# Optimization experiments

Measured on AMD Instinct MI355X. Metric: run time of the kernel, lower is better.

The kernel has to match this reference:

```python
import jax, jax.numpy as jnp
import numpy as np

N_NODES = 50000
N_EDGES = 800000
IN_F = 128
OUT_F = 128
EDGE_F = 6


def setup_inputs() -> dict:
    key = jax.random.key(0)
    k1, k2, k3, k4, k5, k6, k7 = jax.random.split(key, 7)
    nodeFeatures = jax.random.normal(k1, (N_NODES, IN_F), dtype=jnp.float32)
    edgeIndex = jax.random.randint(k2, (N_EDGES, 2), 0, N_NODES, dtype=jnp.int64)
    edgeFeatures = jax.random.normal(k3, (N_EDGES, EDGE_F), dtype=jnp.float32)
    # nn.Linear params (kaiming-uniform-ish init scale)
    lim_n = 1.0 / np.sqrt(IN_F)
    lim_e = 1.0 / np.sqrt(EDGE_F)
    W = jax.random.uniform(k4, (IN_F, OUT_F), minval=-lim_n, maxval=lim_n, dtype=jnp.float32)
    b = jax.random.uniform(k5, (OUT_F,), minval=-lim_n, maxval=lim_n, dtype=jnp.float32)
    We = jax.random.uniform(k6, (EDGE_F, OUT_F), minval=-lim_e, maxval=lim_e, dtype=jnp.float32)
    be = jax.random.uniform(k7, (OUT_F,), minval=-lim_e, maxval=lim_e, dtype=jnp.float32)
    return {"nodeFeatures": nodeFeatures, "edgeIndex": edgeIndex,
            "edgeFeatures": edgeFeatures, "W": W, "b": b, "We": We, "be": be}


def reference(nodeFeatures, edgeIndex, edgeFeatures, W, b, We, be):
    # node linear: [N, out]
    transformed = nodeFeatures @ W + b
    # edge linear: [E, out]
    edgeMsg = edgeFeatures @ We + be
    src = edgeIndex[:, 0]
    dst = edgeIndex[:, 1]
    # per-edge message = transformed[src] + edgeMsg, scatter-add into dst
    messages = transformed[src] + edgeMsg  # [E, out]
    aggregated = jax.ops.segment_sum(messages, dst, num_segments=nodeFeatures.shape[0])
    return jax.nn.relu(aggregated)
```

## Files before the change

kernel.cpp:

```cpp
#include <hip/hip_runtime.h>
#include <hip/hip_bf16.h>
#include <stdint.h>

#define IN_F 128
#define EDGE_F 6
#define TILE_E 4096
#define NBIN_PAD 256

using bf16x8 = __attribute__((ext_vector_type(8))) short;
using f32x4  = __attribute__((ext_vector_type(4))) float;

__device__ __forceinline__ float bf2f(unsigned short u) {
    return __uint_as_float(((unsigned int)u) << 16);
}
__device__ __forceinline__ unsigned short f2bfbits(float f) {
    __hip_bfloat16 h = __float2bfloat16(f);
    return *reinterpret_cast<unsigned short*>(&h);
}
__device__ __forceinline__ unsigned int packbf(float a, float b) {
    return ((unsigned int)f2bfbits(b) << 16) | (unsigned int)f2bfbits(a);
}

__global__ __launch_bounds__(256) void pack_hist_cast(
        const int* __restrict__ eidx, const float* __restrict__ ef,
        uint4* __restrict__ efp, unsigned short* __restrict__ pmat,
        int n_edges, int nblk_e, int n_cast, int eb,
        const float* __restrict__ nf, unsigned short* __restrict__ nfb,
        const float* __restrict__ W, const float* __restrict__ b,
        const float* __restrict__ We, const float* __restrict__ be,
        unsigned short* __restrict__ Wpack, float* __restrict__ W2pack) {
    const int tid = threadIdx.x;
    const int blk = blockIdx.x;
    __shared__ int hist[NBIN_PAD];

    if (blk == eb) {
        for (int idx = tid; idx < 16384; idx += 256) {
            int j = idx & 7, lane = (idx >> 3) & 63, ft = (idx >> 9) & 7, kb = idx >> 12;
            int k = kb * 32 + (lane >> 4) * 8 + j;
            int f = ft * 16 + (lane & 15);
            Wpack[idx] = f2bfbits(W[k * 128 + f]);
        }
        for (int idx = tid; idx < 1024; idx += 256) {
            int j = idx >> 7, f = idx & 127;
            float w = 0.f;
            if (j < 6)       w = We[j * 128 + f];
            else if (j == 6) w = b[f] + be[f];
            W2pack[idx] = w;
        }
    } else {
        const bool hb = (blk < nblk_e);
        if (hb) {
            hist[tid] = 0;
            __syncthreads();
        }
        const int t = blk * 256 + tid;
        if (t < n_edges) {
            const int2 pr = reinterpret_cast<const int2*>(eidx)[t];
            const float2* efs = reinterpret_cast<const float2*>(ef + (size_t)t * EDGE_F);
            const float2 f0 = efs[0], f1 = efs[1], f2 = efs[2];
            uint4 q;
            q.x = (unsigned int)pr.x | ((unsigned int)pr.y << 16);
            q.y = packbf(f0.x, f0.y);
            q.z = packbf(f1.x, f1.y);
            q.w = packbf(f2.x, f2.y);
            efp[t] = q;
        }
        if (hb) {
            const int e0 = blk * TILE_E;
#pragma unroll
            for (int i = 0; i < TILE_E / 256; ++i) {
                const int e = e0 + i * 256 + tid;
                if (e < n_edges) {
                    const int dst = reinterpret_cast<const int2*>(eidx)[e].y;
                    atomicAdd(&hist[dst >> 8], 1);
                }
            }
            __syncthreads();
            pmat[(size_t)blk * NBIN_PAD + tid] = (unsigned short)hist[tid];
        }
    }
    const int t = blk * 256 + tid;
    const int stride = gridDim.x * 256;
    for (int i = t; i < n_cast; i += stride) {
        const float4 lo = reinterpret_cast<const float4*>(nf)[2 * i];
        const float4 hi = reinterpret_cast<const float4*>(nf)[2 * i + 1];
        uint4 o;
        o.x = packbf(lo.x, lo.y); o.y = packbf(lo.z, lo.w);
        o.z = packbf(hi.x, hi.y); o.w = packbf(hi.z, hi.w);
        reinterpret_cast<uint4*>(nfb)[i] = o;
    }
}

__global__ __launch_bounds__(256) void coarse_scatter(
        const uint4* __restrict__ efp, const unsigned short* __restrict__ pmat,
        uint4* __restrict__ rec_c, int* __restrict__ gbase,
        int n_edges, int nblk_e, int nbin) {
    const int tid = threadIdx.x;
    const int blk = blockIdx.x;
    __shared__ int cur[NBIN_PAD];
    __shared__ int sc[NBIN_PAD];
    int tot = 0, pre = 0;
#pragma unroll 4
    for (int bb = 0; bb < nblk_e; ++bb) {
        const int v = pmat[(size_t)bb * NBIN_PAD + tid];
        tot += v;
        pre += (bb < blk) ? v : 0;
    }
    sc[tid] = tot;
    __syncthreads();
    for (int off = 1; off < 256; off <<= 1) {
        int t2 = (tid >= off) ? sc[tid - off] : 0;
        __syncthreads();
        sc[tid] += t2;
        __syncthreads();
    }
    const int excl = sc[tid] - tot;
    cur[tid] = excl + pre;
    if (blk == 0 && tid <= nbin) gbase[tid] = excl;
    __syncthreads();
    const int e0 = blk * TILE_E;
#pragma unroll
    for (int i = 0; i < TILE_E / 256; ++i) {
        const int e = e0 + i * 256 + tid;
        if (e < n_edges) {
            const uint4 q = efp[e];
            const int cb = q.x >> 24;
            const int pos = atomicAdd(&cur[cb], 1);
            rec_c[pos] = q;
        }
    }
}

__global__ __launch_bounds__(256) void fine_rank(
        const uint4* __restrict__ rec_c, const int* __restrict__ gbase,
        uint4* __restrict__ rec, int* __restrict__ rowptr, int n_nodes) {
    const int tid = threadIdx.x;
    const int c = blockIdx.x;
    const int rbase = gbase[c], rend = gbase[c + 1];
    __shared__ int fcnt[256];
    __shared__ int fpos[256];
    fcnt[tid] = 0;
    __syncthreads();
    for (int i = rbase + tid; i < rend; i += 256) {
        const unsigned int qx = reinterpret_cast<const unsigned int*>(rec_c)[(size_t)i * 4];
        atomicAdd(&fcnt[(qx >> 16) & 255], 1);
    }
    __syncthreads();
    const int own = fcnt[tid];
    for (int off = 1; off < 256; off <<= 1) {
        int t2 = (tid >= off) ? fcnt[tid - off] : 0;
        __syncthreads();
        fcnt[tid] += t2;
        __syncthreads();
    }
    const int excl = fcnt[tid] - own;
    fpos[tid] = excl;
    const int n = c * 256 + tid;
    if (n <= n_nodes) rowptr[n] = rbase + excl;
    if (c == 0 && tid == 0) rowptr[n_nodes] = gbase[gridDim.x];
    __syncthreads();
    for (int i = rbase + tid; i < rend; i += 256) {
        const uint4 q = rec_c[i];
        const int r = atomicAdd(&fpos[(q.x >> 16) & 255], 1);
        rec[rbase + r] = q;
    }
}

__global__ __launch_bounds__(256) void aggregate_bf16(
        const unsigned short* __restrict__ nfb, const uint4* __restrict__ rec,
        const int* __restrict__ rowptr, unsigned short* __restrict__ S,
        unsigned short* __restrict__ E8, int n_nodes) {
    const int lane = threadIdx.x & 63;
    const int wv = __builtin_amdgcn_readfirstlane(threadIdx.x >> 6);
    const int n = blockIdx.x * 4 + wv;
    if (n >= n_nodes) return;
    const int r0 = rowptr[n], r1 = rowptr[n + 1];
    const int deg = r1 - r0;
    float ax = 0.f, ay = 0.f;
    float e0 = 0.f, e1 = 0.f, e2 = 0.f, e3 = 0.f, e4 = 0.f, e5 = 0.f;
    int i = r0;
    for (; i + 7 < r1; i += 8) {
        uint4 q[8];
        unsigned int u[8];
#pragma unroll
        for (int j = 0; j < 8; ++j) q[j] = rec[i + j];
#pragma unroll
        for (int j = 0; j < 8; ++j)
            u[j] = reinterpret_cast<const unsigned int*>(nfb + (size_t)(q[j].x & 0xFFFFu) * IN_F)[lane];
#pragma unroll
        for (int j = 0; j < 8; ++j) {
            ax += bf2f((unsigned short)u[j]);
            ay += bf2f((unsigned short)(u[j] >> 16));
            e0 += bf2f((unsigned short)q[j].y);
            e1 += bf2f((unsigned short)(q[j].y >> 16));
            e2 += bf2f((unsigned short)q[j].z);
            e3 += bf2f((unsigned short)(q[j].z >> 16));
            e4 += bf2f((unsigned short)q[j].w);
            e5 += bf2f((unsigned short)(q[j].w >> 16));
        }
    }
    for (; i + 3 < r1; i += 4) {
        uint4 q[4];
        unsigned int u[4];
#pragma unroll
        for (int j = 0; j < 4; ++j) q[j] = rec[i + j];
#pragma unroll
        for (int j = 0; j < 4; ++j)
            u[j] = reinterpret_cast<const unsigned int*>(nfb + (size_t)(q[j].x & 0xFFFFu) * IN_F)[lane];
#pragma unroll
        for (int j = 0; j < 4; ++j) {
            ax += bf2f((unsigned short)u[j]);
            ay += bf2f((unsigned short)(u[j] >> 16));
            e0 += bf2f((unsigned short)q[j].y);
            e1 += bf2f((unsigned short)(q[j].y >> 16));
            e2 += bf2f((unsigned short)q[j].z);
            e3 += bf2f((unsigned short)(q[j].z >> 16));
            e4 += bf2f((unsigned short)q[j].w);
            e5 += bf2f((unsigned short)(q[j].w >> 16));
        }
    }
    for (; i < r1; ++i) {
        const uint4 q0 = rec[i];
        const unsigned int u0 = reinterpret_cast<const unsigned int*>(nfb + (size_t)(q0.x & 0xFFFFu) * IN_F)[lane];
        ax += bf2f((unsigned short)u0); ay += bf2f((unsigned short)(u0 >> 16));
        e0 += bf2f((unsigned short)q0.y); e1 += bf2f((unsigned short)(q0.y >> 16));
        e2 += bf2f((unsigned short)q0.z); e3 += bf2f((unsigned short)(q0.z >> 16));
        e4 += bf2f((unsigned short)q0.w); e5 += bf2f((unsigned short)(q0.w >> 16));
    }
    unsigned short* row = S + (size_t)n * IN_F;
    reinterpret_cast<unsigned int*>(row)[lane] = packbf(ax, ay);
    if (lane == 0) {
        uint4 q;
        q.x = packbf(e0, e1);
        q.y = packbf(e2, e3);
        q.z = packbf(e4, e5);
        q.w = packbf((float)deg, 0.f);
        *reinterpret_cast<uint4*>(E8 + (size_t)n * 8) = q;
    }
}

__global__ __launch_bounds__(256) void gemm_mfma(
        const unsigned short* __restrict__ S, const unsigned short* __restrict__ E8,
        const unsigned short* __restrict__ Wpack, const float* __restrict__ W2pack,
        float* __restrict__ out, int n_nodes) {
    __shared__ __align__(16) short Wl[16384];
    __shared__ float W2l[1024];
    const int tid = threadIdx.x;
    for (int i = tid; i < 2048; i += 256)
        reinterpret_cast<uint4*>(Wl)[i] = reinterpret_cast<const uint4*>(Wpack)[i];
    for (int i = tid; i < 1024; i += 256) W2l[i] = W2pack[i];

    const int wv = tid >> 6, lane = tid & 63;
    const int m = lane & 15, quad = lane >> 4;
    const int n0 = blockIdx.x * 64 + wv * 16;

    const int arow = min(n0 + m, n_nodes - 1);
    const unsigned short* ap = S + (size_t)arow * IN_F + quad * 8;
    bf16x8 a[4];
#pragma unroll
    for (int kb = 0; kb < 4; ++kb)
        a[kb] = *reinterpret_cast<const bf16x8*>(ap + kb * 32);

    __syncthreads();

    f32x4 acc[8];
#pragma unroll
    for (int ft = 0; ft < 8; ++ft) acc[ft] = (f32x4){0.f, 0.f, 0.f, 0.f};

#pragma unroll
    for (int kb = 0; kb < 4; ++kb) {
#pragma unroll
        for (int ft = 0; ft < 8; ++ft) {
            const bf16x8 bfrag =
                reinterpret_cast<const bf16x8*>(Wl)[(kb * 8 + ft) * 64 + lane];
            acc[ft] = __builtin_amdgcn_mfma_f32_16x16x32_bf16(a[kb], bfrag, acc[ft], 0, 0, 0);
        }
    }

    float e[4][7];
#pragma unroll
    for (int r = 0; r < 4; ++r) {
        const int n = min(n0 + quad * 4 + r, n_nodes - 1);
        const uint4 q = *reinterpret_cast<const uint4*>(E8 + (size_t)n * 8);
        e[r][0] = bf2f((unsigned short)q.x); e[r][1] = bf2f((unsigned short)(q.x >> 16));
        e[r][2] = bf2f((unsigned short)q.y); e[r][3] = bf2f((unsigned short)(q.y >> 16));
        e[r][4] = bf2f((unsigned short)q.z); e[r][5] = bf2f((unsigned short)(q.z >> 16));
        e[r][6] = bf2f((unsigned short)q.w);
    }
#pragma unroll
    for (int ft = 0; ft < 8; ++ft) {
        const int f = ft * 16 + m;
        float w2[7];
#pragma unroll
        for (int j = 0; j < 7; ++j) w2[j] = W2l[j * 128 + f];
#pragma unroll
        for (int r = 0; r < 4; ++r) {
            const int n = n0 + quad * 4 + r;
            if (n < n_nodes) {
                float v = acc[ft][r];
#pragma unroll
                for (int j = 0; j < 7; ++j) v += e[r][j] * w2[j];
                out[(size_t)n * 128 + f] = fmaxf(v, 0.f);
            }
        }
    }
}

extern "C" void kernel_launch(void* const* d_in, const int* in_sizes, int n_in,
                              void* d_out, int out_size, void* d_ws, size_t ws_size,
                              hipStream_t stream) {
    const float* nf = (const float*)d_in[0];
    const int* eidx = (const int*)d_in[1];
    const float* ef = (const float*)d_in[2];
    const float* W  = (const float*)d_in[3];
    const float* b  = (const float*)d_in[4];
    const float* We = (const float*)d_in[5];
    const float* be = (const float*)d_in[6];
    float* out = (float*)d_out;

    const int n_nodes = in_sizes[0] / IN_F;
    const int n_edges = in_sizes[1] / 2;

    const int eb = (n_edges + 255) / 256;
    const int nblk_e = (n_edges + TILE_E - 1) / TILE_E;
    const int nbin = (n_nodes + 255) >> 8;
    const int n_cast = n_nodes * (IN_F / 8);

    uint4* rec   = (uint4*)d_ws;
    uint4* efp   = rec + n_edges;
    uint4* rec_c = efp + n_edges;
    unsigned short* S = (unsigned short*)(rec_c + n_edges);
    unsigned short* E8 = S + (size_t)n_nodes * IN_F;
    unsigned short* Wpack = E8 + (size_t)n_nodes * 8;
    float* W2pack = (float*)(Wpack + 16384);
    unsigned short* pmat = (unsigned short*)(W2pack + 1024);
    int* gbase  = (int*)(pmat + (size_t)nblk_e * NBIN_PAD);
    int* rowptr = gbase + 260;
    const int rp_pad = (n_nodes + 1 + 3) & ~3;
    unsigned short* nfb = (unsigned short*)(rowptr + rp_pad);

    pack_hist_cast<<<eb + 1, 256, 0, stream>>>(eidx, ef, efp, pmat,
                                               n_edges, nblk_e, n_cast, eb,
                                               nf, nfb, W, b, We, be, Wpack, W2pack);
    coarse_scatter<<<nblk_e, 256, 0, stream>>>(efp, pmat, rec_c, gbase,
                                               n_edges, nblk_e, nbin);
    fine_rank<<<nbin, 256, 0, stream>>>(rec_c, gbase, rec, rowptr, n_nodes);
    aggregate_bf16<<<(n_nodes + 3) / 4, 256, 0, stream>>>(nfb, rec, rowptr, S, E8, n_nodes);
    gemm_mfma<<<(n_nodes + 63) / 64, 256, 0, stream>>>(S, E8, Wpack, W2pack, out, n_nodes);
}
```

Measured before the change: 194.2 us.

## Fuse fine ranking into aggregation using shared-memory edge index lists

Merges the fine_rank and aggregate kernels into one fine_agg kernel. Each coarse bin of 256 nodes is split across 8 blocks, and each block builds a shared-memory list of 16-bit edge offsets for its 32 nodes. It then gathers rec_c records through those indices instead of writing a fully sorted rec array plus rowptr. This removes one kernel launch and a full global write and read of the 800K sorted records. In exchange, every block rescans the whole bin's record headers twice, and there is a slow fallback path when a block's edge count exceeds the index-buffer capacity.

```diff
diff --git a/kernel.cpp b/kernel.cpp
--- a/kernel.cpp
+++ b/kernel.cpp
@@ -6,6 +6,8 @@
 #define EDGE_F 6
 #define TILE_E 4096
 #define NBIN_PAD 256
+#define SPLIT 8
+#define IDXCAP 1280
 
 using bf16x8 = __attribute__((ext_vector_type(8))) short;
 using f32x4  = __attribute__((ext_vector_type(4))) float;
@@ -131,111 +133,144 @@
     }
 }
 
-__global__ __launch_bounds__(256) void fine_rank(
+__global__ __launch_bounds__(256) void fine_agg(
         const uint4* __restrict__ rec_c, const int* __restrict__ gbase,
-        uint4* __restrict__ rec, int* __restrict__ rowptr, int n_nodes) {
+        const unsigned short* __restrict__ nfb,
+        unsigned short* __restrict__ S, unsigned short* __restrict__ E8,
+        int n_nodes) {
     const int tid = threadIdx.x;
-    const int c = blockIdx.x;
+    const int c = blockIdx.x / SPLIT;
+    const int part = blockIdx.x % SPLIT;
     const int rbase = gbase[c], rend = gbase[c + 1];
-    __shared__ int fcnt[256];
-    __shared__ int fpos[256];
-    fcnt[tid] = 0;
-    __syncthreads();
-    for (int i = rbase + tid; i < rend; i += 256) {
-        const unsigned int qx = reinterpret_cast<const unsigned int*>(rec_c)[(size_t)i * 4];
-        atomicAdd(&fcnt[(qx >> 16) & 255], 1);
-    }
-    __syncthreads();
-    const int own = fcnt[tid];
-    for (int off = 1; off < 256; off <<= 1) {
-        int t2 = (tid >= off) ? fcnt[tid - off] : 0;
+    const int sz = rend - rbase;
+    __shared__ int scnt[32];
+    __shared__ int spos[32];
+    __shared__ int sok;
+    __shared__ unsigned short sidx[IDXCAP];
+    if (tid < 32) scnt[tid] = 0;
+    __syncthreads();
+    for (int i = tid; i < sz; i += 256) {
+        const unsigned int qx =
+            reinterpret_cast<const unsigned int*>(rec_c)[(size_t)(rbase + i) * 4];
+        const int d = (qx >> 16) & 255;
+        if ((d >> 5) == part) atomicAdd(&scnt[d & 31], 1);
+    }
+    __syncthreads();
+    if (tid == 0) {
+        int run = 0;
+        for (int j = 0; j < 32; ++j) { spos[j] = run; run += scnt[j]; }
+        sok = (run <= IDXCAP && sz <= 65535) ? 1 : 0;
+    }
+    __syncthreads();
+    const int ok = sok;
+    if (ok) {
+        for (int i = tid; i < sz; i += 256) {
+            const unsigned int qx =
+                reinterpret_cast<const unsigned int*>(rec_c)[(size_t)(rbase + i) * 4];
+            const int d = (qx >> 16) & 255;
+            if ((d >> 5) == part) {
+                const int r = atomicAdd(&spos[d & 31], 1);
+                sidx[r] = (unsigned short)i;
+            }
+        }
         __syncthreads();
-        fcnt[tid] += t2;
-        __syncthreads();
-    }
-    const int excl = fcnt[tid] - own;
-    fpos[tid] = excl;
-    const int n = c * 256 + tid;
-    if (n <= n_nodes) rowptr[n] = rbase + excl;
-    if (c == 0 && tid == 0) rowptr[n_nodes] = gbase[gridDim.x];
-    __syncthreads();
-    for (int i = rbase + tid; i < rend; i += 256) {
-        const uint4 q = rec_c[i];
-        const int r = atomicAdd(&fpos[(q.x >> 16) & 255], 1);
-        rec[rbase + r] = q;
-    }
-}
-
-__global__ __launch_bounds__(256) void aggregate_bf16(
-        const unsigned short* __restrict__ nfb, const uint4* __restrict__ rec,
-        const int* __restrict__ rowptr, unsigned short* __restrict__ S,
-        unsigned short* __restrict__ E8, int n_nodes) {
-    const int lane = threadIdx.x & 63;
-    const int wv = __builtin_amdgcn_readfirstlane(threadIdx.x >> 6);
-    const int n = blockIdx.x * 4 + wv;
-    if (n >= n_nodes) return;
-    const int r0 = rowptr[n], r1 = rowptr[n + 1];
-    const int deg = r1 - r0;
-    float ax = 0.f, ay = 0.f;
-    float e0 = 0.f, e1 = 0.f, e2 = 0.f, e3 = 0.f, e4 = 0.f, e5 = 0.f;
-    int i = r0;
-    for (; i + 7 < r1; i += 8) {
-        uint4 q[8];
-        unsigned int u[8];
-#pragma unroll
-        for (int j = 0; j < 8; ++j) q[j] = rec[i + j];
-#pragma unroll
-        for (int j = 0; j < 8; ++j)
-            u[j] = reinterpret_cast<const unsigned int*>(nfb + (size_t)(q[j].x & 0xFFFFu) * IN_F)[lane];
-#pragma unroll
-        for (int j = 0; j < 8; ++j) {
-            ax += bf2f((unsigned short)u[j]);
-            ay += bf2f((unsigned short)(u[j] >> 16));
-            e0 += bf2f((unsigned short)q[j].y);
-            e1 += bf2f((unsigned short)(q[j].y >> 16));
-            e2 += bf2f((unsigned short)q[j].z);
-            e3 += bf2f((unsigned short)(q[j].z >> 16));
-            e4 += bf2f((unsigned short)q[j].w);
-            e5 += bf2f((unsigned short)(q[j].w >> 16));
-        }
-    }
-    for (; i + 3 < r1; i += 4) {
-        uint4 q[4];
-        unsigned int u[4];
-#pragma unroll
-        for (int j = 0; j < 4; ++j) q[j] = rec[i + j];
-#pragma unroll
-        for (int j = 0; j < 4; ++j)
-            u[j] = reinterpret_cast<const unsigned int*>(nfb + (size_t)(q[j].x & 0xFFFFu) * IN_F)[lane];
-#pragma unroll
-        for (int j = 0; j < 4; ++j) {
-            ax += bf2f((unsigned short)u[j]);
-            ay += bf2f((unsigned short)(u[j] >> 16));
-            e0 += bf2f((unsigned short)q[j].y);
-            e1 += bf2f((unsigned short)(q[j].y >> 16));
-            e2 += bf2f((unsigned short)q[j].z);
-            e3 += bf2f((unsigned short)(q[j].z >> 16));
-            e4 += bf2f((unsigned short)q[j].w);
-            e5 += bf2f((unsigned short)(q[j].w >> 16));
-        }
-    }
-    for (; i < r1; ++i) {
-        const uint4 q0 = rec[i];
-        const unsigned int u0 = reinterpret_cast<const unsigned int*>(nfb + (size_t)(q0.x & 0xFFFFu) * IN_F)[lane];
-        ax += bf2f((unsigned short)u0); ay += bf2f((unsigned short)(u0 >> 16));
-        e0 += bf2f((unsigned short)q0.y); e1 += bf2f((unsigned short)(q0.y >> 16));
-        e2 += bf2f((unsigned short)q0.z); e3 += bf2f((unsigned short)(q0.z >> 16));
-        e4 += bf2f((unsigned short)q0.w); e5 += bf2f((unsigned short)(q0.w >> 16));
-    }
-    unsigned short* row = S + (size_t)n * IN_F;
-    reinterpret_cast<unsigned int*>(row)[lane] = packbf(ax, ay);
-    if (lane == 0) {
-        uint4 q;
-        q.x = packbf(e0, e1);
-        q.y = packbf(e2, e3);
-        q.z = packbf(e4, e5);
-        q.w = packbf((float)deg, 0.f);
-        *reinterpret_cast<uint4*>(E8 + (size_t)n * 8) = q;
+    }
+    const int lane = tid & 63;
+    const int wv = tid >> 6;
+#pragma unroll 1
+    for (int k = 0; k < 8; ++k) {
+        const int dl = part * 32 + wv * 8 + k;
+        const int n = c * 256 + dl;
+        if (n >= n_nodes) continue;
+        float ax = 0.f, ay = 0.f;
+        float e0 = 0.f, e1 = 0.f, e2 = 0.f, e3 = 0.f, e4 = 0.f, e5 = 0.f;
+        int deg = 0;
+        if (ok) {
+            const int cnt = scnt[dl & 31];
+            const int start = spos[dl & 31] - cnt;
+            deg = cnt;
+            int j = 0;
+            for (; j + 7 < cnt; j += 8) {
+                int ei[8]; uint4 q[8]; unsigned int u[8];
+#pragma unroll
+                for (int t2 = 0; t2 < 8; ++t2)
+                    ei[t2] = __builtin_amdgcn_readfirstlane(rbase + (int)sidx[start + j + t2]);
+#pragma unroll
+                for (int t2 = 0; t2 < 8; ++t2) q[t2] = rec_c[ei[t2]];
+#pragma unroll
+                for (int t2 = 0; t2 < 8; ++t2)
+                    u[t2] = reinterpret_cast<const unsigned int*>(
+                        nfb + (size_t)(q[t2].x & 0xFFFFu) * IN_F)[lane];
+#pragma unroll
+                for (int t2 = 0; t2 < 8; ++t2) {
+                    ax += bf2f((unsigned short)u[t2]);
+                    ay += bf2f((unsigned short)(u[t2] >> 16));
+                    e0 += bf2f((unsigned short)q[t2].y);
+                    e1 += bf2f((unsigned short)(q[t2].y >> 16));
+                    e2 += bf2f((unsigned short)q[t2].z);
+                    e3 += bf2f((unsigned short)(q[t2].z >> 16));
+                    e4 += bf2f((unsigned short)q[t2].w);
+                    e5 += bf2f((unsigned short)(q[t2].w >> 16));
+                }
+            }
+            for (; j + 3 < cnt; j += 4) {
+                int ei[4]; uint4 q[4]; unsigned int u[4];
+#pragma unroll
+                for (int t2 = 0; t2 < 4; ++t2)
+                    ei[t2] = __builtin_amdgcn_readfirstlane(rbase + (int)sidx[start + j + t2]);
+#pragma unroll
+                for (int t2 = 0; t2 < 4; ++t2) q[t2] = rec_c[ei[t2]];
+#pragma unroll
+                for (int t2 = 0; t2 < 4; ++t2)
+                    u[t2] = reinterpret_cast<const unsigned int*>(
+                        nfb + (size_t)(q[t2].x & 0xFFFFu) * IN_F)[lane];
+#pragma unroll
+                for (int t2 = 0; t2 < 4; ++t2) {
+                    ax += bf2f((unsigned short)u[t2]);
+                    ay += bf2f((unsigned short)(u[t2] >> 16));
+                    e0 += bf2f((unsigned short)q[t2].y);
+                    e1 += bf2f((unsigned short)(q[t2].y >> 16));
+                    e2 += bf2f((unsigned short)q[t2].z);
+                    e3 += bf2f((unsigned short)(q[t2].z >> 16));
+                    e4 += bf2f((unsigned short)q[t2].w);
+                    e5 += bf2f((unsigned short)(q[t2].w >> 16));
+                }
+            }
+            for (; j < cnt; ++j) {
+                const int e = __builtin_amdgcn_readfirstlane(rbase + (int)sidx[start + j]);
+                const uint4 q0 = rec_c[e];
+                const unsigned int u0 = reinterpret_cast<const unsigned int*>(
+                    nfb + (size_t)(q0.x & 0xFFFFu) * IN_F)[lane];
+                ax += bf2f((unsigned short)u0); ay += bf2f((unsigned short)(u0 >> 16));
+                e0 += bf2f((unsigned short)q0.y); e1 += bf2f((unsigned short)(q0.y >> 16));
+                e2 += bf2f((unsigned short)q0.z); e3 += bf2f((unsigned short)(q0.z >> 16));
+                e4 += bf2f((unsigned short)q0.w); e5 += bf2f((unsigned short)(q0.w >> 16));
+            }
+        } else {
+            for (int i2 = 0; i2 < sz; ++i2) {
+                const int e = __builtin_amdgcn_readfirstlane(rbase + i2);
+                const uint4 q0 = rec_c[e];
+                if ((int)((q0.x >> 16) & 255) == dl) {
+                    const unsigned int u0 = reinterpret_cast<const unsigned int*>(
+                        nfb + (size_t)(q0.x & 0xFFFFu) * IN_F)[lane];
+                    ax += bf2f((unsigned short)u0); ay += bf2f((unsigned short)(u0 >> 16));
+                    e0 += bf2f((unsigned short)q0.y); e1 += bf2f((unsigned short)(q0.y >> 16));
+                    e2 += bf2f((unsigned short)q0.z); e3 += bf2f((unsigned short)(q0.z >> 16));
+                    e4 += bf2f((unsigned short)q0.w); e5 += bf2f((unsigned short)(q0.w >> 16));
+                    ++deg;
+                }
+            }
+        }
+        unsigned short* row = S + (size_t)n * IN_F;
+        reinterpret_cast<unsigned int*>(row)[lane] = packbf(ax, ay);
+        if (lane == 0) {
+            uint4 qq;
+            qq.x = packbf(e0, e1);
+            qq.y = packbf(e2, e3);
+            qq.z = packbf(e4, e5);
+            qq.w = packbf((float)deg, 0.f);
+            *reinterpret_cast<uint4*>(E8 + (size_t)n * 8) = qq;
+        }
     }
 }
 
@@ -326,25 +361,21 @@
     const int nbin = (n_nodes + 255) >> 8;
     const int n_cast = n_nodes * (IN_F / 8);
 
-    uint4* rec   = (uint4*)d_ws;
-    uint4* efp   = rec + n_edges;
+    uint4* efp   = (uint4*)d_ws;
     uint4* rec_c = efp + n_edges;
     unsigned short* S = (unsigned short*)(rec_c + n_edges);
     unsigned short* E8 = S + (size_t)n_nodes * IN_F;
     unsigned short* Wpack = E8 + (size_t)n_nodes * 8;
     float* W2pack = (float*)(Wpack + 16384);
     unsigned short* pmat = (unsigned short*)(W2pack + 1024);
-    int* gbase  = (int*)(pmat + (size_t)nblk_e * NBIN_PAD);
-    int* rowptr = gbase + 260;
-    const int rp_pad = (n_nodes + 1 + 3) & ~3;
-    unsigned short* nfb = (unsigned short*)(rowptr + rp_pad);
+    int* gbase = (int*)(pmat + (size_t)nblk_e * NBIN_PAD);
+    unsigned short* nfb = (unsigned short*)(gbase + 260);
 
     pack_hist_cast<<<eb + 1, 256, 0, stream>>>(eidx, ef, efp, pmat,
                                                n_edges, nblk_e, n_cast, eb,
                                                nf, nfb, W, b, We, be, Wpack, W2pack);
     coarse_scatter<<<nblk_e, 256, 0, stream>>>(efp, pmat, rec_c, gbase,
                                                n_edges, nblk_e, nbin);
-    fine_rank<<<nbin, 256, 0, stream>>>(rec_c, gbase, rec, rowptr, n_nodes);
-    aggregate_bf16<<<(n_nodes + 3) / 4, 256, 0, stream>>>(nfb, rec, rowptr, S, E8, n_nodes);
+    fine_agg<<<nbin * SPLIT, 256, 0, stream>>>(rec_c, gbase, nfb, S, E8, n_nodes);
     gemm_mfma<<<(n_nodes + 63) / 64, 256, 0, stream>>>(S, E8, Wpack, W2pack, out, n_nodes);
 }
```

After: 219.3 us. 12.9% more time.

## Pad each node's CSR segment to multiples of eight with dummy records

Applied to the files above, without the earlier changes.

Fine ranking now rounds each node's edge count up to a multiple of eight. It writes dummy records that point at a zeroed extra row appended to the bf16 node features, and stores a (start, degree) pair per node instead of a rowptr. Aggregation then runs only the unrolled 8-wide loop, dropping the 4-wide and scalar tail loops and their divergence. In exchange it gathers and reads extra padding records, about 3.5 per node on average, and relies on a fixed per-bin pad budget (PADMAX) that must cover 256 nodes' worth of padding.

```diff
diff --git a/kernel.cpp b/kernel.cpp
--- a/kernel.cpp
+++ b/kernel.cpp
@@ -6,6 +6,7 @@
 #define EDGE_F 6
 #define TILE_E 4096
 #define NBIN_PAD 256
+#define PADMAX 1792
 
 using bf16x8 = __attribute__((ext_vector_type(8))) short;
 using f32x4  = __attribute__((ext_vector_type(4))) float;
@@ -24,7 +25,7 @@
 __global__ __launch_bounds__(256) void pack_hist_cast(
         const int* __restrict__ eidx, const float* __restrict__ ef,
         uint4* __restrict__ efp, unsigned short* __restrict__ pmat,
-        int n_edges, int nblk_e, int n_cast, int eb,
+        int n_edges, int nblk_e, int n_cast, int eb, int n_nodes,
         const float* __restrict__ nf, unsigned short* __restrict__ nfb,
         const float* __restrict__ W, const float* __restrict__ b,
         const float* __restrict__ We, const float* __restrict__ be,
@@ -46,6 +47,10 @@
             if (j < 6)       w = We[j * 128 + f];
             else if (j == 6) w = b[f] + be[f];
             W2pack[idx] = w;
+        }
+        if (tid < 16) {
+            uint4 z; z.x = z.y = z.z = z.w = 0u;
+            reinterpret_cast<uint4*>(nfb + (size_t)n_nodes * IN_F)[tid] = z;
         }
     } else {
         const bool hb = (blk < nblk_e);
@@ -133,10 +138,11 @@
 
 __global__ __launch_bounds__(256) void fine_rank(
         const uint4* __restrict__ rec_c, const int* __restrict__ gbase,
-        uint4* __restrict__ rec, int* __restrict__ rowptr, int n_nodes) {
+        uint4* __restrict__ rec, int2* __restrict__ pr2, int n_nodes) {
     const int tid = threadIdx.x;
     const int c = blockIdx.x;
     const int rbase = gbase[c], rend = gbase[c + 1];
+    const int pbase = rbase + c * PADMAX;
     __shared__ int fcnt[256];
     __shared__ int fpos[256];
     fcnt[tid] = 0;
@@ -147,46 +153,56 @@
     }
     __syncthreads();
     const int own = fcnt[tid];
+    const int ownp = (own + 7) & ~7;
+    fcnt[tid] = ownp;
+    __syncthreads();
     for (int off = 1; off < 256; off <<= 1) {
         int t2 = (tid >= off) ? fcnt[tid - off] : 0;
         __syncthreads();
         fcnt[tid] += t2;
         __syncthreads();
     }
-    const int excl = fcnt[tid] - own;
-    fpos[tid] = excl;
+    const int pexcl = fcnt[tid] - ownp;
+    fpos[tid] = pexcl;
     const int n = c * 256 + tid;
-    if (n <= n_nodes) rowptr[n] = rbase + excl;
-    if (c == 0 && tid == 0) rowptr[n_nodes] = gbase[gridDim.x];
+    if (n < n_nodes) {
+        int2 pr; pr.x = pbase + pexcl; pr.y = own;
+        pr2[n] = pr;
+    }
     __syncthreads();
     for (int i = rbase + tid; i < rend; i += 256) {
         const uint4 q = rec_c[i];
         const int r = atomicAdd(&fpos[(q.x >> 16) & 255], 1);
-        rec[rbase + r] = q;
-    }
+        rec[pbase + r] = q;
+    }
+    uint4 dmy; dmy.x = (unsigned int)n_nodes; dmy.y = dmy.z = dmy.w = 0u;
+    for (int j = own; j < ownp; ++j)
+        rec[pbase + pexcl + j] = dmy;
 }
 
 __global__ __launch_bounds__(256) void aggregate_bf16(
         const unsigned short* __restrict__ nfb, const uint4* __restrict__ rec,
-        const int* __restrict__ rowptr, unsigned short* __restrict__ S,
+        const int2* __restrict__ pr2, unsigned short* __restrict__ S,
         unsigned short* __restrict__ E8, int n_nodes) {
     const int lane = threadIdx.x & 63;
     const int wv = __builtin_amdgcn_readfirstlane(threadIdx.x >> 6);
     const int n = blockIdx.x * 4 + wv;
     if (n >= n_nodes) return;
-    const int r0 = rowptr[n], r1 = rowptr[n + 1];
-    const int deg = r1 - r0;
+    const int2 pr = pr2[n];
+    const int deg = pr.y;
+    const int nb = (deg + 7) >> 3;
     float ax = 0.f, ay = 0.f;
     float e0 = 0.f, e1 = 0.f, e2 = 0.f, e3 = 0.f, e4 = 0.f, e5 = 0.f;
-    int i = r0;
-    for (; i + 7 < r1; i += 8) {
+    int i = pr.x;
+    for (int bb = 0; bb < nb; ++bb, i += 8) {
         uint4 q[8];
         unsigned int u[8];
 #pragma unroll
         for (int j = 0; j < 8; ++j) q[j] = rec[i + j];
 #pragma unroll
         for (int j = 0; j < 8; ++j)
-            u[j] = reinterpret_cast<const unsigned int*>(nfb + (size_t)(q[j].x & 0xFFFFu) * IN_F)[lane];
+            u[j] = reinterpret_cast<const unsigned int*>(
+                nfb + (size_t)(q[j].x & 0xFFFFu) * IN_F)[lane];
 #pragma unroll
         for (int j = 0; j < 8; ++j) {
             ax += bf2f((unsigned short)u[j]);
@@ -198,34 +214,6 @@
             e4 += bf2f((unsigned short)q[j].w);
             e5 += bf2f((unsigned short)(q[j].w >> 16));
         }
-    }
-    for (; i + 3 < r1; i += 4) {
-        uint4 q[4];
-        unsigned int u[4];
-#pragma unroll
-        for (int j = 0; j < 4; ++j) q[j] = rec[i + j];
-#pragma unroll
-        for (int j = 0; j < 4; ++j)
-            u[j] = reinterpret_cast<const unsigned int*>(nfb + (size_t)(q[j].x & 0xFFFFu) * IN_F)[lane];
-#pragma unroll
-        for (int j = 0; j < 4; ++j) {
-            ax += bf2f((unsigned short)u[j]);
-            ay += bf2f((unsigned short)(u[j] >> 16));
-            e0 += bf2f((unsigned short)q[j].y);
-            e1 += bf2f((unsigned short)(q[j].y >> 16));
-            e2 += bf2f((unsigned short)q[j].z);
-            e3 += bf2f((unsigned short)(q[j].z >> 16));
-            e4 += bf2f((unsigned short)q[j].w);
-            e5 += bf2f((unsigned short)(q[j].w >> 16));
-        }
-    }
-    for (; i < r1; ++i) {
-        const uint4 q0 = rec[i];
-        const unsigned int u0 = reinterpret_cast<const unsigned int*>(nfb + (size_t)(q0.x & 0xFFFFu) * IN_F)[lane];
-        ax += bf2f((unsigned short)u0); ay += bf2f((unsigned short)(u0 >> 16));
-        e0 += bf2f((unsigned short)q0.y); e1 += bf2f((unsigned short)(q0.y >> 16));
-        e2 += bf2f((unsigned short)q0.z); e3 += bf2f((unsigned short)(q0.z >> 16));
-        e4 += bf2f((unsigned short)q0.w); e5 += bf2f((unsigned short)(q0.w >> 16));
     }
     unsigned short* row = S + (size_t)n * IN_F;
     reinterpret_cast<unsigned int*>(row)[lane] = packbf(ax, ay);
@@ -327,24 +315,23 @@
     const int n_cast = n_nodes * (IN_F / 8);
 
     uint4* rec   = (uint4*)d_ws;
-    uint4* efp   = rec + n_edges;
+    uint4* efp   = rec + ((size_t)n_edges + (size_t)nbin * PADMAX);
     uint4* rec_c = efp + n_edges;
     unsigned short* S = (unsigned short*)(rec_c + n_edges);
     unsigned short* E8 = S + (size_t)n_nodes * IN_F;
     unsigned short* Wpack = E8 + (size_t)n_nodes * 8;
     float* W2pack = (float*)(Wpack + 16384);
     unsigned short* pmat = (unsigned short*)(W2pack + 1024);
-    int* gbase  = (int*)(pmat + (size_t)nblk_e * NBIN_PAD);
-    int* rowptr = gbase + 260;
-    const int rp_pad = (n_nodes + 1 + 3) & ~3;
-    unsigned short* nfb = (unsigned short*)(rowptr + rp_pad);
+    int* gbase = (int*)(pmat + (size_t)nblk_e * NBIN_PAD);
+    int2* pr2 = (int2*)(gbase + 260);
+    unsigned short* nfb = (unsigned short*)(pr2 + n_nodes);
 
     pack_hist_cast<<<eb + 1, 256, 0, stream>>>(eidx, ef, efp, pmat,
-                                               n_edges, nblk_e, n_cast, eb,
+                                               n_edges, nblk_e, n_cast, eb, n_nodes,
                                                nf, nfb, W, b, We, be, Wpack, W2pack);
     coarse_scatter<<<nblk_e, 256, 0, stream>>>(efp, pmat, rec_c, gbase,
                                                n_edges, nblk_e, nbin);
-    fine_rank<<<nbin, 256, 0, stream>>>(rec_c, gbase, rec, rowptr, n_nodes);
-    aggregate_bf16<<<(n_nodes + 3) / 4, 256, 0, stream>>>(nfb, rec, rowptr, S, E8, n_nodes);
+    fine_rank<<<nbin, 256, 0, stream>>>(rec_c, gbase, rec, pr2, n_nodes);
+    aggregate_bf16<<<(n_nodes + 3) / 4, 256, 0, stream>>>(nfb, rec, pr2, S, E8, n_nodes);
     gemm_mfma<<<(n_nodes + 63) / 64, 256, 0, stream>>>(S, E8, Wpack, W2pack, out, n_nodes);
 }
```

Measured after the change: 194.8 us. About the same (+0.3%).
